# Performance work log

Hardware: AMD Instinct MI355X
Metric: run time of the kernel (lower is better)

Reference implementation:

```python
import jax, jax.numpy as jnp
import numpy as np

N_NODES = 100000
N_EDGES = 3200000
IN_DIM = 256


def gcn_conv(x, src, dst, W, b):
    # PyG GCNConv: add self-loops, symmetric normalization D^-1/2 A D^-1/2
    n = x.shape[0]
    loop = jnp.arange(n)
    s = jnp.concatenate([src, loop])
    d = jnp.concatenate([dst, loop])
    deg = jax.ops.segment_sum(jnp.ones(d.shape, x.dtype), d, num_segments=n)
    dinv = jnp.where(deg > 0, jax.lax.rsqrt(deg), 0.0).astype(x.dtype)
    norm = dinv[s] * dinv[d]                      # [E+N]
    h = x @ W                                     # [N, out] transform first (out < in)
    msg = h[s] * norm[:, None]                    # gather + scale
    out = jax.ops.segment_sum(msg, d, num_segments=n)  # scatter-add
    return out + b


def setup_inputs() -> dict:
    key = jax.random.key(0)
    ks = jax.random.split(key, 8)
    x = jax.random.normal(ks[0], (N_NODES, IN_DIM), dtype=jnp.float32)
    edge_index = jax.random.randint(ks[1], (2, N_EDGES), 0, N_NODES, dtype=jnp.int64)
    # Glorot-ish scaled params
    W1 = jax.random.normal(ks[2], (IN_DIM, 64), dtype=jnp.float32) / np.sqrt(IN_DIM)
    b1 = jnp.zeros((64,), jnp.float32)
    W2 = jax.random.normal(ks[3], (64, 32), dtype=jnp.float32) / np.sqrt(64)
    b2 = jnp.zeros((32,), jnp.float32)
    fc_w = jax.random.normal(ks[4], (1, 32), dtype=jnp.float32) / np.sqrt(32)
    fc_b = jnp.zeros((1,), jnp.float32)
    return {"x": x, "edge_index": edge_index, "W1": W1, "b1": b1,
            "W2": W2, "b2": b2, "fc_w": fc_w, "fc_b": fc_b}


def reference(x, edge_index, W1, b1, W2, b2, fc_w, fc_b):
    src, dst = edge_index[0], edge_index[1]
    h = jax.nn.relu(gcn_conv(x, src, dst, W1, b1))   # [N, 64]
    h = jax.nn.relu(gcn_conv(h, src, dst, W2, b2))   # [N, 32]
    pooled = h.mean(axis=0)                          # [32]
    return pooled @ fc_w.T + fc_b                    # [1]
```

## Files before the change

### kernel.cpp

```cpp
#include <hip/hip_runtime.h>
#include <hip/hip_fp16.h>

#ifndef F1
#define F1 64
#define F2 32
#endif

#define NBLK 512
#define BSH  7
#define BNODES 128
#define CAP  5120

typedef _Float16 half8 __attribute__((ext_vector_type(8)));
typedef float floatx4 __attribute__((ext_vector_type(4)));


__global__ __launch_bounds__(256) void prep_kernel(const float* __restrict__ W1,
                                                   const float* __restrict__ W2,
                                                   __half* __restrict__ W1t,
                                                   __half* __restrict__ W2t,
                                                   float* __restrict__ out,
                                                   int* __restrict__ cnt, int NB) {
    if (threadIdx.x == 0) out[0] = 0.f;
    for (int i = threadIdx.x; i < NB; i += 256) cnt[i] = 0;
    for (int e = threadIdx.x; e < 64 * 256; e += 256) {
        int n = e >> 8, k = e & 255;
        W1t[e] = __float2half(W1[k * 64 + n]);
    }
    for (int e = threadIdx.x; e < 32 * 64; e += 256) {
        int n = e >> 6, k = e & 63;
        W2t[e] = __float2half(W2[k * 32 + n]);
    }
}


__global__ __launch_bounds__(256) void bucket_scatter2(const int* __restrict__ src,
                                                       const int* __restrict__ dst,
                                                       int* __restrict__ cnt,
                                                       int* __restrict__ buck,
                                                       int E, int CH, int NB) {
    __shared__ int lcnt[1024];
    __shared__ int cur[1024];
    int b = blockIdx.x;
    int tid = threadIdx.x;
    for (int i = tid; i < NB; i += 256) lcnt[i] = 0;
    __syncthreads();
    int start = b * CH, end = min(E, start + CH);
    for (int e0 = start + tid * 4; e0 < end; e0 += 1024) {
        if (e0 + 4 <= end) {
            int4 d4 = *reinterpret_cast<const int4*>(dst + e0);
            atomicAdd(&lcnt[d4.x >> BSH], 1);
            atomicAdd(&lcnt[d4.y >> BSH], 1);
            atomicAdd(&lcnt[d4.z >> BSH], 1);
            atomicAdd(&lcnt[d4.w >> BSH], 1);
        } else {
            for (int e = e0; e < end; ++e) atomicAdd(&lcnt[dst[e] >> BSH], 1);
        }
    }
    __syncthreads();
    for (int i = tid; i < NB; i += 256) {
        int c = lcnt[i];
        cur[i] = (c > 0) ? (i * CAP + atomicAdd(&cnt[i], c)) : 0;
    }
    __syncthreads();
    for (int e0 = start + tid * 4; e0 < end; e0 += 1024) {
        if (e0 + 4 <= end) {
            int4 s4 = *reinterpret_cast<const int4*>(src + e0);
            int4 d4 = *reinterpret_cast<const int4*>(dst + e0);
            int p0 = atomicAdd(&cur[d4.x >> BSH], 1);
            buck[p0] = (s4.x << BSH) | (d4.x & (BNODES - 1));
            int p1 = atomicAdd(&cur[d4.y >> BSH], 1);
            buck[p1] = (s4.y << BSH) | (d4.y & (BNODES - 1));
            int p2 = atomicAdd(&cur[d4.z >> BSH], 1);
            buck[p2] = (s4.z << BSH) | (d4.z & (BNODES - 1));
            int p3 = atomicAdd(&cur[d4.w >> BSH], 1);
            buck[p3] = (s4.w << BSH) | (d4.w & (BNODES - 1));
        } else {
            for (int e = e0; e < end; ++e) {
                int d = dst[e];
                int pos = atomicAdd(&cur[d >> BSH], 1);
                buck[pos] = (src[e] << BSH) | (d & (BNODES - 1));
            }
        }
    }
}


__global__ __launch_bounds__(256) void bucket_deg_fill2(const int* __restrict__ buck,
                                                        const int* __restrict__ cnt,
                                                        int* __restrict__ deg,
                                                        float* __restrict__ dinv,
                                                        int* __restrict__ row_off,
                                                        int* __restrict__ csr,
                                                        int N, int NB) {
    __shared__ int bcnt[BNODES];
    __shared__ int sc[BNODES];
    __shared__ int lrow[BNODES];
    __shared__ int lcur[BNODES];
    int k = blockIdx.x;
    int tid = threadIdx.x;
    if (tid < BNODES) { bcnt[tid] = 0; lcur[tid] = 0; }
    __syncthreads();
    int bs = k * CAP;
    int be = bs + cnt[k];
    for (int e = bs + tid; e < be; e += 256)
        atomicAdd(&bcnt[buck[e] & (BNODES - 1)], 1);
    __syncthreads();
    if (tid < BNODES) sc[tid] = bcnt[tid];
    __syncthreads();
    for (int ofs = 1; ofs < BNODES; ofs <<= 1) {
        int v = (tid >= ofs && tid < BNODES) ? sc[tid - ofs] : 0;
        __syncthreads();
        if (tid < BNODES) sc[tid] += v;
        __syncthreads();
    }
    if (tid < BNODES) {
        int excl = sc[tid] - bcnt[tid];
        lrow[tid] = bs + excl;
        int i = (k << BSH) + tid;
        if (i < N) {
            deg[i] = bcnt[tid];
            dinv[i] = rsqrtf((float)(bcnt[tid] + 1));
            row_off[i] = bs + excl;
        }
    }
    __syncthreads();
    for (int e = bs + tid; e < be; e += 256) {
        int p = buck[e];
        int li = p & (BNODES - 1);
        int pos = lrow[li] + atomicAdd(&lcur[li], 1);
        csr[pos] = p >> BSH;
    }
}


__device__ __forceinline__ int swz(int p, int r) { return (p ^ ((r >> 1) & 3)) << 4; }

template <bool AF32, int K, int BN>
__global__ __launch_bounds__(256) void gemm_mfma_kernel(const void* __restrict__ Aptr,
                                                        const __half* __restrict__ Bt,
                                                        const float* __restrict__ dinv,
                                                        __half* __restrict__ C,
                                                        int M) {
    constexpr int NT = BN / 16;
    __shared__ half8 Ash[64 * 4];
    __shared__ half8 Bsh[BN * 4];
    char* Ab = (char*)Ash;
    char* Bb = (char*)Bsh;
    int tid = threadIdx.x;
    int w = tid >> 6;
    int l = tid & 63;
    int row0 = blockIdx.x * 64;
    int sr = tid >> 2, sp = tid & 3;
    int fr = l & 15, fp = l >> 4;
    int arow = w * 16 + fr;
    int a_off = arow * 64 + swz(fp, arow);

    floatx4 acc[NT];
#pragma unroll
    for (int c = 0; c < NT; ++c) acc[c] = (floatx4){0.f, 0.f, 0.f, 0.f};

    for (int k0 = 0; k0 < K; k0 += 32) {
        half8 av = {};
        int gr = row0 + sr;
        if (gr < M) {
            if constexpr (AF32) {
                const float* A = (const float*)Aptr;
                float4 f0 = *(const float4*)(A + (size_t)gr * K + k0 + sp * 8);
                float4 f1 = *(const float4*)(A + (size_t)gr * K + k0 + sp * 8 + 4);
                av[0] = (_Float16)f0.x; av[1] = (_Float16)f0.y;
                av[2] = (_Float16)f0.z; av[3] = (_Float16)f0.w;
                av[4] = (_Float16)f1.x; av[5] = (_Float16)f1.y;
                av[6] = (_Float16)f1.z; av[7] = (_Float16)f1.w;
            } else {
                const __half* A = (const __half*)Aptr;
                av = *(const half8*)(A + (size_t)gr * K + k0 + sp * 8);
            }
        }
        *(half8*)(Ab + sr * 64 + swz(sp, sr)) = av;
        if (tid < BN * 4) {
            int n = tid >> 2, p = tid & 3;
            half8 bv = *(const half8*)(Bt + (size_t)n * K + k0 + p * 8);
            *(half8*)(Bb + n * 64 + swz(p, n)) = bv;
        }
        __syncthreads();
        half8 a = *(const half8*)(Ab + a_off);
#pragma unroll
        for (int c = 0; c < NT; ++c) {
            int col = c * 16 + fr;
            half8 b = *(const half8*)(Bb + col * 64 + swz(fp, col));
            acc[c] = __builtin_amdgcn_mfma_f32_16x16x32_f16(a, b, acc[c], 0, 0, 0);
        }
        __syncthreads();
    }
#pragma unroll
    for (int i = 0; i < 4; ++i) {
        int r = row0 + w * 16 + fp * 4 + i;
        if (r < M) {
            float dn = dinv[r];
#pragma unroll
            for (int c = 0; c < NT; ++c)
                C[(size_t)r * BN + c * 16 + fr] = __float2half(acc[c][i] * dn);
        }
    }
}


__device__ __forceinline__ void acc_row16(const __half* __restrict__ base, float* a) {
    uint4 raw = *reinterpret_cast<const uint4*>(base);
    float2 f0 = __half22float2(*reinterpret_cast<const __half2*>(&raw.x));
    float2 f1 = __half22float2(*reinterpret_cast<const __half2*>(&raw.y));
    float2 f2 = __half22float2(*reinterpret_cast<const __half2*>(&raw.z));
    float2 f3 = __half22float2(*reinterpret_cast<const __half2*>(&raw.w));
    a[0] += f0.x; a[1] += f0.y; a[2] += f1.x; a[3] += f1.y;
    a[4] += f2.x; a[5] += f2.y; a[6] += f3.x; a[7] += f3.y;
}

__device__ __forceinline__ void acc_pk_raw(uint4 raw, __half2* c2) {
    c2[0] = __hadd2(c2[0], *reinterpret_cast<const __half2*>(&raw.x));
    c2[1] = __hadd2(c2[1], *reinterpret_cast<const __half2*>(&raw.y));
    c2[2] = __hadd2(c2[2], *reinterpret_cast<const __half2*>(&raw.z));
    c2[3] = __hadd2(c2[3], *reinterpret_cast<const __half2*>(&raw.w));
}

__device__ __forceinline__ void flush_pk(__half2* c2, float* a) {
#pragma unroll
    for (int j = 0; j < 4; ++j) {
        float2 f = __half22float2(c2[j]);
        a[2 * j] += f.x;
        a[2 * j + 1] += f.y;
        c2[j] = __float2half2_rn(0.f);
    }
}


__global__ __launch_bounds__(256) void agg1_kernel(const __half* __restrict__ g1,
                                                   const int* __restrict__ row_off,
                                                   const int* __restrict__ deg,
                                                   const int* __restrict__ csr,
                                                   const float* __restrict__ dinv,
                                                   const float* __restrict__ b1,
                                                   __half* __restrict__ h1, int n) {
    int node = (blockIdx.x * 256 + threadIdx.x) >> 6;
    int lane = threadIdx.x & 63;
    int g = lane >> 3;
    int f8 = lane & 7;
    if (node >= n) return;
    int start = row_off[node];
    int end = start + deg[node];
    float a[8];
#pragma unroll
    for (int j = 0; j < 8; ++j) a[j] = 0.f;
    if (g == 0)
        acc_row16(g1 + ((size_t)node << 6) + f8 * 8, a);
    __half2 c2[4];
#pragma unroll
    for (int j = 0; j < 4; ++j) c2[j] = __float2half2_rn(0.f);
    int e = start;
    for (; e + 32 <= end; e += 32) {
        int i0 = csr[e + g];
        int i1 = csr[e + 8 + g];
        int i2 = csr[e + 16 + g];
        int i3 = csr[e + 24 + g];
        uint4 r0 = *reinterpret_cast<const uint4*>(g1 + ((size_t)i0 << 6) + f8 * 8);
        uint4 r1 = *reinterpret_cast<const uint4*>(g1 + ((size_t)i1 << 6) + f8 * 8);
        uint4 r2 = *reinterpret_cast<const uint4*>(g1 + ((size_t)i2 << 6) + f8 * 8);
        uint4 r3 = *reinterpret_cast<const uint4*>(g1 + ((size_t)i3 << 6) + f8 * 8);
        acc_pk_raw(r0, c2);
        acc_pk_raw(r1, c2);
        acc_pk_raw(r2, c2);
        acc_pk_raw(r3, c2);
        flush_pk(c2, a);
    }
    if (e + 16 <= end) {
        int i0 = csr[e + g];
        int i1 = csr[e + 8 + g];
        uint4 r0 = *reinterpret_cast<const uint4*>(g1 + ((size_t)i0 << 6) + f8 * 8);
        uint4 r1 = *reinterpret_cast<const uint4*>(g1 + ((size_t)i1 << 6) + f8 * 8);
        acc_pk_raw(r0, c2);
        acc_pk_raw(r1, c2);
        e += 16;
    }
    if (e + 8 <= end) {
        int s = csr[e + g];
        uint4 r = *reinterpret_cast<const uint4*>(g1 + ((size_t)s << 6) + f8 * 8);
        acc_pk_raw(r, c2);
        e += 8;
    }
    if (e + g < end) {
        int s = csr[e + g];
        uint4 r = *reinterpret_cast<const uint4*>(g1 + ((size_t)s << 6) + f8 * 8);
        acc_pk_raw(r, c2);
    }
    flush_pk(c2, a);
#pragma unroll
    for (int j = 0; j < 8; ++j) a[j] += __shfl_xor(a[j], 8);
#pragma unroll
    for (int j = 0; j < 8; ++j) a[j] += __shfl_xor(a[j], 16);
#pragma unroll
    for (int j = 0; j < 8; ++j) a[j] += __shfl_xor(a[j], 32);
    if (g == 0) {
        float dn = dinv[node];
        float4 bl = *reinterpret_cast<const float4*>(b1 + f8 * 8);
        float4 bh = *reinterpret_cast<const float4*>(b1 + f8 * 8 + 4);
        __half hh[8];
        hh[0] = __float2half(fmaxf(a[0] * dn + bl.x, 0.f));
        hh[1] = __float2half(fmaxf(a[1] * dn + bl.y, 0.f));
        hh[2] = __float2half(fmaxf(a[2] * dn + bl.z, 0.f));
        hh[3] = __float2half(fmaxf(a[3] * dn + bl.w, 0.f));
        hh[4] = __float2half(fmaxf(a[4] * dn + bh.x, 0.f));
        hh[5] = __float2half(fmaxf(a[5] * dn + bh.y, 0.f));
        hh[6] = __float2half(fmaxf(a[6] * dn + bh.z, 0.f));
        hh[7] = __float2half(fmaxf(a[7] * dn + bh.w, 0.f));
        *reinterpret_cast<uint4*>(h1 + ((size_t)node << 6) + f8 * 8) =
            *reinterpret_cast<const uint4*>(hh);
    }
}


__global__ __launch_bounds__(256) void agg2_pool_kernel(const __half* __restrict__ g2,
                                                        const int* __restrict__ row_off,
                                                        const int* __restrict__ deg,
                                                        const int* __restrict__ csr,
                                                        const float* __restrict__ dinv,
                                                        const float* __restrict__ b2,
                                                        float* __restrict__ partials,
                                                        int nblocks, int n) {
    int tid = threadIdx.x;
    int half = tid >> 5;
    int node = blockIdx.x * 8 + half;
    int l32 = tid & 31;
    int g = (l32 >> 2);
    int f4 = l32 & 3;
    float a[8];
#pragma unroll
    for (int j = 0; j < 8; ++j) a[j] = 0.f;
    if (node < n) {
        int start = row_off[node];
        int end = start + deg[node];
        if (g == 0)
            acc_row16(g2 + ((size_t)node << 5) + f4 * 8, a);
        __half2 c2[4];
#pragma unroll
        for (int j = 0; j < 4; ++j) c2[j] = __float2half2_rn(0.f);
        int e = start;
        for (; e + 32 <= end; e += 32) {
            int i0 = csr[e + g];
            int i1 = csr[e + 8 + g];
            int i2 = csr[e + 16 + g];
            int i3 = csr[e + 24 + g];
            uint4 r0 = *reinterpret_cast<const uint4*>(g2 + ((size_t)i0 << 5) + f4 * 8);
            uint4 r1 = *reinterpret_cast<const uint4*>(g2 + ((size_t)i1 << 5) + f4 * 8);
            uint4 r2 = *reinterpret_cast<const uint4*>(g2 + ((size_t)i2 << 5) + f4 * 8);
            uint4 r3 = *reinterpret_cast<const uint4*>(g2 + ((size_t)i3 << 5) + f4 * 8);
            acc_pk_raw(r0, c2);
            acc_pk_raw(r1, c2);
            acc_pk_raw(r2, c2);
            acc_pk_raw(r3, c2);
            flush_pk(c2, a);
        }
        if (e + 16 <= end) {
            int i0 = csr[e + g];
            int i1 = csr[e + 8 + g];
            uint4 r0 = *reinterpret_cast<const uint4*>(g2 + ((size_t)i0 << 5) + f4 * 8);
            uint4 r1 = *reinterpret_cast<const uint4*>(g2 + ((size_t)i1 << 5) + f4 * 8);
            acc_pk_raw(r0, c2);
            acc_pk_raw(r1, c2);
            e += 16;
        }
        if (e + 8 <= end) {
            int s = csr[e + g];
            uint4 r = *reinterpret_cast<const uint4*>(g2 + ((size_t)s << 5) + f4 * 8);
            acc_pk_raw(r, c2);
            e += 8;
        }
        if (e + g < end) {
            int s = csr[e + g];
            uint4 r = *reinterpret_cast<const uint4*>(g2 + ((size_t)s << 5) + f4 * 8);
            acc_pk_raw(r, c2);
        }
        flush_pk(c2, a);
#pragma unroll
        for (int j = 0; j < 8; ++j) a[j] += __shfl_xor(a[j], 4);
#pragma unroll
        for (int j = 0; j < 8; ++j) a[j] += __shfl_xor(a[j], 8);
#pragma unroll
        for (int j = 0; j < 8; ++j) a[j] += __shfl_xor(a[j], 16);
    }
    __shared__ float sdata[8][32];
    if (g == 0) {
        float relu[8];
        if (node < n) {
            float dn = dinv[node];
#pragma unroll
            for (int j = 0; j < 8; ++j)
                relu[j] = fmaxf(a[j] * dn + b2[f4 * 8 + j], 0.f);
        } else {
#pragma unroll
            for (int j = 0; j < 8; ++j) relu[j] = 0.f;
        }
#pragma unroll
        for (int j = 0; j < 8; ++j) sdata[half][f4 * 8 + j] = relu[j];
    }
    __syncthreads();
    if (tid < 32) {
        float s = 0.f;
#pragma unroll
        for (int r = 0; r < 8; ++r) s += sdata[r][tid];
        partials[tid * nblocks + blockIdx.x] = s;
    }
}

__global__ __launch_bounds__(256) void reduce_fc_kernel(const float* __restrict__ partials,
                                                        int nblocks,
                                                        const float* __restrict__ fcw,
                                                        const float* __restrict__ fcb,
                                                        float* __restrict__ out, int n) {
    int f = blockIdx.x;
    const float* col = partials + (size_t)f * nblocks;
    float s = 0.f;
    for (int i = threadIdx.x; i < nblocks; i += 256) s += col[i];
    __shared__ float red[256];
    red[threadIdx.x] = s;
    __syncthreads();
    for (int ofs = 128; ofs > 0; ofs >>= 1) {
        if (threadIdx.x < ofs) red[threadIdx.x] += red[threadIdx.x + ofs];
        __syncthreads();
    }
    if (threadIdx.x == 0) {
        float v = (float)((double)red[0] / (double)n * (double)fcw[f]);
        if (f == 0) v += fcb[0];
        atomicAdd(out, v);
    }
}


extern "C" void kernel_launch(void* const* d_in, const int* in_sizes, int n_in,
                              void* d_out, int out_size, void* d_ws, size_t ws_size,
                              hipStream_t stream) {
    const float* x   = (const float*)d_in[0];
    const int*   ei  = (const int*)d_in[1];
    const float* W1  = (const float*)d_in[2];
    const float* b1  = (const float*)d_in[3];
    const float* W2  = (const float*)d_in[4];
    const float* b2  = (const float*)d_in[5];
    const float* fcw = (const float*)d_in[6];
    const float* fcb = (const float*)d_in[7];
    float* out = (float*)d_out;

    const int N = in_sizes[0] / 256;
    const int E = in_sizes[1] / 2;
    const int* src = ei;
    const int* dst = ei + E;

    const int NB = (N + BNODES - 1) >> BSH;
    const int CH = (((E + NBLK - 1) / NBLK) + 3) & ~3;
    const int nb2 = (N + 7) / 8;
    const size_t CAPTOT = (size_t)NB * CAP;

    char* ws = (char*)d_ws;
    size_t off = 0;
    auto alloc = [&](size_t bytes) -> void* {
        void* p = ws + off;
        off = (off + bytes + 255) & ~(size_t)255;
        return p;
    };
    int*   cnt      = (int*)alloc((size_t)NB * 4);
    int*   row_off  = (int*)alloc((size_t)N * 4);
    int*   deg      = (int*)alloc((size_t)N * 4);
    float* dinv     = (float*)alloc((size_t)N * 4);
    int*   csr      = (int*)alloc(CAPTOT * 4);
    __half* W1t     = (__half*)alloc((size_t)64 * 256 * 2);
    __half* W2t     = (__half*)alloc((size_t)32 * 64 * 2);
    size_t szP = CAPTOT * 4;
    size_t szG1 = (size_t)N * F1 * 2;
    void* P = alloc(szP > szG1 ? szP : szG1);
    int*    buck = (int*)P;
    __half* g1   = (__half*)P;
    __half* h1      = (__half*)alloc((size_t)N * F1 * 2);
    __half* g2      = (__half*)alloc((size_t)N * F2 * 2);
    float* partials = (float*)alloc((size_t)F2 * nb2 * 4);

    prep_kernel<<<1, 256, 0, stream>>>(W1, W2, W1t, W2t, out, cnt, NB);
    bucket_scatter2<<<NBLK, 256, 0, stream>>>(src, dst, cnt, buck, E, CH, NB);
    bucket_deg_fill2<<<NB, 256, 0, stream>>>(buck, cnt, deg, dinv, row_off, csr, N, NB);

    int nbG = (N + 63) / 64;
    gemm_mfma_kernel<true, 256, 64><<<nbG, 256, 0, stream>>>(x, W1t, dinv, g1, N);
    agg1_kernel<<<(N + 3) / 4, 256, 0, stream>>>(g1, row_off, deg, csr, dinv, b1, h1, N);

    gemm_mfma_kernel<false, 64, 32><<<nbG, 256, 0, stream>>>(h1, W2t, dinv, g2, N);
    agg2_pool_kernel<<<nb2, 256, 0, stream>>>(g2, row_off, deg, csr, dinv, b2, partials, nb2, N);

    reduce_fc_kernel<<<F2, 256, 0, stream>>>(partials, nb2, fcw, fcb, out, N);
}
```

Measured before the change: 211.3 us.

## Locally sort edge chunks in LDS before writing buckets to global memory

The bucket scatter kernel now builds a per-block histogram and prefix sum, places each edge into a shared-memory sorted array by destination bucket, and then writes to global buckets in contiguous runs rather than scattered single-word stores. The weight transpose/convert work moves from the single-block prep kernel into an extra block of the scatter kernel, so the serial prep kernel only zeroes counters. This is meant to improve write coalescing in the bucket pass and shorten the serial prep launch. In exchange it adds a 1024-entry scan and about 37 KB of shared memory per block, which can lower occupancy.

Result: faster. 194.5 us (median of 2 runs) (-8.0%).

```diff
diff --git a/kernel.cpp b/kernel.cpp
--- a/kernel.cpp
+++ b/kernel.cpp
@@ -10,78 +10,109 @@
 #define BSH  7
 #define BNODES 128
 #define CAP  5120
+#define CHMAX 6272
 
 typedef _Float16 half8 __attribute__((ext_vector_type(8)));
 typedef float floatx4 __attribute__((ext_vector_type(4)));
 
 
-__global__ __launch_bounds__(256) void prep_kernel(const float* __restrict__ W1,
-                                                   const float* __restrict__ W2,
-                                                   __half* __restrict__ W1t,
-                                                   __half* __restrict__ W2t,
-                                                   float* __restrict__ out,
-                                                   int* __restrict__ cnt, int NB) {
+__global__ __launch_bounds__(256) void prep0_kernel(float* __restrict__ out,
+                                                    int* __restrict__ cnt, int NB) {
     if (threadIdx.x == 0) out[0] = 0.f;
     for (int i = threadIdx.x; i < NB; i += 256) cnt[i] = 0;
-    for (int e = threadIdx.x; e < 64 * 256; e += 256) {
-        int n = e >> 8, k = e & 255;
-        W1t[e] = __float2half(W1[k * 64 + n]);
-    }
-    for (int e = threadIdx.x; e < 32 * 64; e += 256) {
-        int n = e >> 6, k = e & 63;
-        W2t[e] = __float2half(W2[k * 32 + n]);
-    }
-}
-
-
-__global__ __launch_bounds__(256) void bucket_scatter2(const int* __restrict__ src,
+}
+
+
+__global__ __launch_bounds__(256) void scatter_sorted3(const int* __restrict__ src,
                                                        const int* __restrict__ dst,
                                                        int* __restrict__ cnt,
                                                        int* __restrict__ buck,
+                                                       const float* __restrict__ W1,
+                                                       const float* __restrict__ W2,
+                                                       __half* __restrict__ W1t,
+                                                       __half* __restrict__ W2t,
                                                        int E, int CH, int NB) {
-    __shared__ int lcnt[1024];
-    __shared__ int cur[1024];
     int b = blockIdx.x;
     int tid = threadIdx.x;
-    for (int i = tid; i < NB; i += 256) lcnt[i] = 0;
+    if (b == NBLK) {
+        for (int e = tid; e < 64 * 256; e += 256) {
+            int n = e >> 8, k = e & 255;
+            W1t[e] = __float2half(W1[k * 64 + n]);
+        }
+        for (int e = tid; e < 32 * 64; e += 256) {
+            int n = e >> 6, k = e & 63;
+            W2t[e] = __float2half(W2[k * 32 + n]);
+        }
+        return;
+    }
+    __shared__ int gbase[1024];
+    __shared__ int lhist[1024];
+    __shared__ int sc[1024];
+    __shared__ int lcur[1024];
+    __shared__ int sorted[CHMAX];
+    __shared__ unsigned short sbkt[CHMAX];
+    for (int i = tid; i < 1024; i += 256) lhist[i] = 0;
     __syncthreads();
     int start = b * CH, end = min(E, start + CH);
+    int count = end - start;
     for (int e0 = start + tid * 4; e0 < end; e0 += 1024) {
         if (e0 + 4 <= end) {
             int4 d4 = *reinterpret_cast<const int4*>(dst + e0);
-            atomicAdd(&lcnt[d4.x >> BSH], 1);
-            atomicAdd(&lcnt[d4.y >> BSH], 1);
-            atomicAdd(&lcnt[d4.z >> BSH], 1);
-            atomicAdd(&lcnt[d4.w >> BSH], 1);
+            atomicAdd(&lhist[d4.x >> BSH], 1);
+            atomicAdd(&lhist[d4.y >> BSH], 1);
+            atomicAdd(&lhist[d4.z >> BSH], 1);
+            atomicAdd(&lhist[d4.w >> BSH], 1);
         } else {
-            for (int e = e0; e < end; ++e) atomicAdd(&lcnt[dst[e] >> BSH], 1);
-        }
-    }
-    __syncthreads();
-    for (int i = tid; i < NB; i += 256) {
-        int c = lcnt[i];
-        cur[i] = (c > 0) ? (i * CAP + atomicAdd(&cnt[i], c)) : 0;
+            for (int e = e0; e < end; ++e) atomicAdd(&lhist[dst[e] >> BSH], 1);
+        }
+    }
+    __syncthreads();
+    for (int i = tid; i < 1024; i += 256) {
+        int c = lhist[i];
+        gbase[i] = (i < NB && c > 0) ? (i * CAP + atomicAdd(&cnt[i], c)) : 0;
+        sc[i] = c;
+    }
+    __syncthreads();
+    for (int ofs = 1; ofs < 1024; ofs <<= 1) {
+        int i1 = tid + 256, i2 = tid + 512, i3 = tid + 768;
+        int v0 = (tid >= ofs) ? sc[tid - ofs] : 0;
+        int v1 = (i1 >= ofs) ? sc[i1 - ofs] : 0;
+        int v2 = (i2 >= ofs) ? sc[i2 - ofs] : 0;
+        int v3 = (i3 >= ofs) ? sc[i3 - ofs] : 0;
+        __syncthreads();
+        sc[tid] += v0; sc[i1] += v1; sc[i2] += v2; sc[i3] += v3;
+        __syncthreads();
+    }
+    for (int i = tid; i < 1024; i += 256) {
+        int ex = sc[i] - lhist[i];
+        sc[i] = ex;
+        lcur[i] = ex;
     }
     __syncthreads();
     for (int e0 = start + tid * 4; e0 < end; e0 += 1024) {
         if (e0 + 4 <= end) {
             int4 s4 = *reinterpret_cast<const int4*>(src + e0);
             int4 d4 = *reinterpret_cast<const int4*>(dst + e0);
-            int p0 = atomicAdd(&cur[d4.x >> BSH], 1);
-            buck[p0] = (s4.x << BSH) | (d4.x & (BNODES - 1));
-            int p1 = atomicAdd(&cur[d4.y >> BSH], 1);
-            buck[p1] = (s4.y << BSH) | (d4.y & (BNODES - 1));
-            int p2 = atomicAdd(&cur[d4.z >> BSH], 1);
-            buck[p2] = (s4.z << BSH) | (d4.z & (BNODES - 1));
-            int p3 = atomicAdd(&cur[d4.w >> BSH], 1);
-            buck[p3] = (s4.w << BSH) | (d4.w & (BNODES - 1));
+            int k0 = d4.x >> BSH, p0 = atomicAdd(&lcur[k0], 1);
+            sorted[p0] = (s4.x << BSH) | (d4.x & (BNODES - 1)); sbkt[p0] = (unsigned short)k0;
+            int k1 = d4.y >> BSH, p1 = atomicAdd(&lcur[k1], 1);
+            sorted[p1] = (s4.y << BSH) | (d4.y & (BNODES - 1)); sbkt[p1] = (unsigned short)k1;
+            int k2 = d4.z >> BSH, p2 = atomicAdd(&lcur[k2], 1);
+            sorted[p2] = (s4.z << BSH) | (d4.z & (BNODES - 1)); sbkt[p2] = (unsigned short)k2;
+            int k3 = d4.w >> BSH, p3 = atomicAdd(&lcur[k3], 1);
+            sorted[p3] = (s4.w << BSH) | (d4.w & (BNODES - 1)); sbkt[p3] = (unsigned short)k3;
         } else {
             for (int e = e0; e < end; ++e) {
                 int d = dst[e];
-                int pos = atomicAdd(&cur[d >> BSH], 1);
-                buck[pos] = (src[e] << BSH) | (d & (BNODES - 1));
+                int k = d >> BSH, p = atomicAdd(&lcur[k], 1);
+                sorted[p] = (src[e] << BSH) | (d & (BNODES - 1)); sbkt[p] = (unsigned short)k;
             }
         }
+    }
+    __syncthreads();
+    for (int p = tid; p < count; p += 256) {
+        int k = sbkt[p];
+        buck[gbase[k] + (p - sc[k])] = sorted[p];
     }
 }
 
@@ -481,8 +512,8 @@
     __half* g2      = (__half*)alloc((size_t)N * F2 * 2);
     float* partials = (float*)alloc((size_t)F2 * nb2 * 4);
 
-    prep_kernel<<<1, 256, 0, stream>>>(W1, W2, W1t, W2t, out, cnt, NB);
-    bucket_scatter2<<<NBLK, 256, 0, stream>>>(src, dst, cnt, buck, E, CH, NB);
+    prep0_kernel<<<1, 256, 0, stream>>>(out, cnt, NB);
+    scatter_sorted3<<<NBLK + 1, 256, 0, stream>>>(src, dst, cnt, buck, W1, W2, W1t, W2t, E, CH, NB);
     bucket_deg_fill2<<<NB, 256, 0, stream>>>(buck, cnt, deg, dinv, row_off, csr, N, NB);
 
     int nbG = (N + 63) / 64;
```
